# Kernel tuning notes

Hardware: AMD Instinct MI355X
Metric: run time of the kernel (lower is better)

## Reference

```python
import jax, jax.numpy as jnp
import numpy as np

B, S, D_MODEL, H, D_KV = 16, 512, 768, 12, 64
EPS = 1e-6
ROPE_THETA = 10000.0


def rms_norm(x, w, eps=EPS):
    var = jnp.mean(jnp.square(x.astype(jnp.float32)), axis=-1, keepdims=True)
    return w * (x * jax.lax.rsqrt(var + eps))


def rotate_half(x):
    x1, x2 = jnp.split(x, 2, axis=-1)
    return jnp.concatenate([-x2, x1], axis=-1)


def build_rope(position_ids, inv_freq):
    # position_ids: [B,S] int; inv_freq: [d_kv/2]
    freqs = position_ids[:, :, None].astype(jnp.float32) * inv_freq[None, None, :]  # [B,S,d/2]
    emb = jnp.concatenate([freqs, freqs], axis=-1)  # [B,S,d_kv]
    return jnp.cos(emb), jnp.sin(emb)


def shape_heads(x, n_heads, d_kv):
    b, s, _ = x.shape
    return x.reshape(b, s, n_heads, d_kv).transpose(0, 2, 1, 3)  # [b,h,s,d]


def attend(h, norm_w, wq, wk, wv, wo, mask, cos=None, sin=None):
    # h: [b,s,d_model]; mask: [b,h,s,s] additive
    normed = rms_norm(h, norm_w)
    q = shape_heads(normed @ wq.T, H, D_KV)
    k = shape_heads(normed @ wk.T, H, D_KV)
    v = shape_heads(normed @ wv.T, H, D_KV)
    if cos is not None:
        c = cos[:, None, :, :]
        s = sin[:, None, :, :]
        q = q * c + rotate_half(q) * s
        k = k * c + rotate_half(k) * s
    # NOTE: kernel has no 1/sqrt(d) scaling
    scores = jnp.einsum('bhqd,bhkd->bhqk', q, k) + mask
    p = jax.nn.softmax(scores, axis=-1)
    out = jnp.einsum('bhqk,bhkd->bhqd', p, v)
    b, _, s, _ = out.shape
    out = out.transpose(0, 2, 1, 3).reshape(b, s, H * D_KV)
    return h + out @ wo.T


def setup_inputs() -> dict:
    key = jax.random.key(0)
    ks = jax.random.split(key, 12)
    scale = 1.0 / np.sqrt(D_MODEL)
    inp = {
        'hidden_states': jax.random.normal(ks[0], (B, S, D_MODEL), dtype=jnp.float32),
        'position_ids': jnp.broadcast_to(jnp.arange(S, dtype=jnp.int32)[None, :], (B, S)),
        'attention_mask': jnp.broadcast_to(
            jnp.where(jnp.arange(S)[None, :] <= jnp.arange(S)[:, None], 0.0, -1e9).astype(jnp.float32),
            (B, H, S, S)) + 0.0,
        'group_time_mask': jnp.zeros((S, H, B, B), dtype=jnp.float32),
        't_q': jax.random.normal(ks[1], (H * D_KV, D_MODEL), dtype=jnp.float32) * scale,
        't_k': jax.random.normal(ks[2], (H * D_KV, D_MODEL), dtype=jnp.float32) * scale,
        't_v': jax.random.normal(ks[3], (H * D_KV, D_MODEL), dtype=jnp.float32) * scale,
        't_o': jax.random.normal(ks[4], (D_MODEL, H * D_KV), dtype=jnp.float32) * scale,
        't_norm_w': jnp.ones((D_MODEL,), dtype=jnp.float32),
        'g_q': jax.random.normal(ks[5], (H * D_KV, D_MODEL), dtype=jnp.float32) * scale,
        'g_k': jax.random.normal(ks[6], (H * D_KV, D_MODEL), dtype=jnp.float32) * scale,
        'g_v': jax.random.normal(ks[7], (H * D_KV, D_MODEL), dtype=jnp.float32) * scale,
        'g_o': jax.random.normal(ks[8], (D_MODEL, H * D_KV), dtype=jnp.float32) * scale,
        'g_norm_w': jnp.ones((D_MODEL,), dtype=jnp.float32),
        'inv_freq': (1.0 / ROPE_THETA ** (jnp.arange(0, D_KV, 2, dtype=jnp.float32) / D_KV)),
    }
    return inp


def reference(hidden_states, position_ids, attention_mask, group_time_mask,
              t_q, t_k, t_v, t_o, t_norm_w,
              g_q, g_k, g_v, g_o, g_norm_w, inv_freq):
    cos, sin = build_rope(position_ids, inv_freq)
    h = attend(hidden_states, t_norm_w, t_q, t_k, t_v, t_o, attention_mask, cos, sin)
    h = h.transpose(1, 0, 2)  # [S,B,D]: group attention attends across groups
    h = attend(h, g_norm_w, g_q, g_k, g_v, g_o, group_time_mask)
    return h.transpose(1, 0, 2)
```

## Files before the change

### kernel.cpp

```cpp
#include <hip/hip_runtime.h>

#define DM   768
#define QKVN 2304
#define SQ   512
#define NB   16
#define NH   12

typedef unsigned short u16;
typedef _Float16 h16;
typedef _Float16 h16x8 __attribute__((ext_vector_type(8)));
typedef float f32x4 __attribute__((ext_vector_type(4)));

__device__ __forceinline__ u16 f2h(float f) {
  h16 h = (h16)f;
  return __builtin_bit_cast(u16, h);
}
__device__ __forceinline__ float h2f(u16 u) {
  return (float)__builtin_bit_cast(h16, u);
}
__device__ __forceinline__ void gload_lds16(const void* g, void* l) {
  __builtin_amdgcn_global_load_lds((__attribute__((address_space(1))) void*)(g),
                                   (__attribute__((address_space(3))) void*)(l), 16, 0, 0);
}

struct WPtrs { const float* s[8]; u16* d[8]; };
__global__ __launch_bounds__(256) void prep_k(WPtrs P, const float* __restrict__ invf,
                                              float* __restrict__ tab,
                                              const float* __restrict__ x, const float* __restrict__ nw,
                                              u16* __restrict__ normed) {
  const int bid = blockIdx.x, tid = threadIdx.x;
  if (bid < 4608) {
    int w = bid / 576;
    int i = ((bid % 576) * 256 + tid) * 4;
    float4 v = *reinterpret_cast<const float4*>(P.s[w] + i);
    ushort4 o;
    o.x = f2h(v.x); o.y = f2h(v.y); o.z = f2h(v.z); o.w = f2h(v.w);
    *reinterpret_cast<ushort4*>(P.d[w] + i) = o;
  } else if (bid < 4672) {
    int i = (bid - 4608) * 256 + tid;
    int pos = i >> 5, j = i & 31;
    float a = (float)pos * invf[j];
    float s, c;
    sincosf(a, &s, &c);
    tab[i * 2] = c; tab[i * 2 + 1] = s;
  } else {
    int wv = tid >> 6, lane = tid & 63;
    size_t t = (size_t)(bid - 4672) * 4 + wv;
    const float* row = x + t * DM;
    float4 v[3];
    float ss = 0.f;
#pragma unroll
    for (int i = 0; i < 3; i++) {
      v[i] = *reinterpret_cast<const float4*>(row + (lane + 64 * i) * 4);
      ss += v[i].x * v[i].x + v[i].y * v[i].y + v[i].z * v[i].z + v[i].w * v[i].w;
    }
#pragma unroll
    for (int d = 1; d < 64; d <<= 1) ss += __shfl_xor(ss, d);
    float rs = rsqrtf(ss * (1.0f / 768.f) + 1e-6f);
    u16* orow = normed + t * DM;
#pragma unroll
    for (int i = 0; i < 3; i++) {
      int c = (lane + 64 * i) * 4;
      float4 wv4 = *reinterpret_cast<const float4*>(nw + c);
      ushort4 o;
      o.x = f2h(v[i].x * rs * wv4.x);
      o.y = f2h(v[i].y * rs * wv4.y);
      o.z = f2h(v[i].z * rs * wv4.z);
      o.w = f2h(v[i].w * rs * wv4.w);
      *reinterpret_cast<ushort4*>(orow + c) = o;
    }
  }
}

__global__ __launch_bounds__(256) void rms_k(const u16* __restrict__ x, const float* __restrict__ w,
                                             u16* __restrict__ out) {
  int wv = threadIdx.x >> 6, lane = threadIdx.x & 63;
  size_t t = (size_t)blockIdx.x * 4 + wv;
  const u16* row = x + t * DM;
  float4 v[3];
  float ss = 0.f;
#pragma unroll
  for (int i = 0; i < 3; i++) {
    ushort4 rw = *reinterpret_cast<const ushort4*>(row + (lane + 64 * i) * 4);
    v[i].x = h2f(rw.x); v[i].y = h2f(rw.y); v[i].z = h2f(rw.z); v[i].w = h2f(rw.w);
    ss += v[i].x * v[i].x + v[i].y * v[i].y + v[i].z * v[i].z + v[i].w * v[i].w;
  }
#pragma unroll
  for (int d = 1; d < 64; d <<= 1) ss += __shfl_xor(ss, d);
  float rs = rsqrtf(ss * (1.0f / 768.f) + 1e-6f);
  u16* orow = out + t * DM;
#pragma unroll
  for (int i = 0; i < 3; i++) {
    int c = (lane + 64 * i) * 4;
    float4 wv4 = *reinterpret_cast<const float4*>(w + c);
    ushort4 o;
    o.x = f2h(v[i].x * rs * wv4.x);
    o.y = f2h(v[i].y * rs * wv4.y);
    o.z = f2h(v[i].z * rs * wv4.z);
    o.w = f2h(v[i].w * rs * wv4.w);
    *reinterpret_cast<ushort4*>(orow + c) = o;
  }
}

template <int CMODE, bool ROPE, int PERM, bool VT>
__global__ __launch_bounds__(256, 3) void gemm_k(const u16* __restrict__ A, const u16* __restrict__ W, int N,
                                              void* __restrict__ C, const void* __restrict__ resid,
                                              const int* __restrict__ pids, const float* __restrict__ tab,
                                              u16* __restrict__ vt) {
  __shared__ __align__(16) char L[3 * 16384];
  const int tid = threadIdx.x, w = tid >> 6, lane = tid & 63;
  const int wr = w >> 1, wc = w & 1;
  const int nbn = gridDim.y;
  int nf = blockIdx.y * gridDim.x + blockIdx.x;
  int nwg = gridDim.x * nbn;
  int swv = (nf & 7) * (nwg >> 3) + (nf >> 3);
  const int bm = swv / nbn;
  const int bnb = swv % nbn;
  const int l15 = lane & 15, l4 = lane >> 4;
  f32x4 acc[4][4] = {};

  const int r0 = tid >> 2, k40 = tid & 3;
  const int k4s = k40 ^ ((r0 >> 1) & 3);
  const size_t aA0 = (size_t)(bm * 128 + r0) * 1536 + k4s * 16;
  const size_t aA1 = (size_t)(bm * 128 + r0 + 64) * 1536 + k4s * 16;
  const size_t aB0 = (size_t)(bnb * 128 + r0) * 1536 + k4s * 16;
  const size_t aB1 = (size_t)(bnb * 128 + r0 + 64) * 1536 + k4s * 16;
  const int dc0 = tid * 16, dc1 = dc0 + 4096;
  const char* Ab = (const char*)A;
  const char* Wb = (const char*)W;

#define STAGE(T64, Q) do { \
    gload_lds16(Ab + aA0 + (T64), L + (Q) * 16384 + dc0); \
    gload_lds16(Ab + aA1 + (T64), L + (Q) * 16384 + dc1); \
    gload_lds16(Wb + aB0 + (T64), L + (Q) * 16384 + 8192 + dc0); \
    gload_lds16(Wb + aB1 + (T64), L + (Q) * 16384 + 8192 + dc1); \
  } while (0)

  int obA[4], obB[4];
#pragma unroll
  for (int i = 0; i < 4; i++) {
    int rowA = wr * 64 + i * 16 + l15;
    obA[i] = rowA * 64 + ((l4 ^ ((rowA >> 1) & 3)) * 16);
    int rowB = wc * 64 + i * 16 + l15;
    obB[i] = 8192 + rowB * 64 + ((l4 ^ ((rowB >> 1) & 3)) * 16);
  }

  STAGE(0, 0); STAGE(64, 1);
  asm volatile("s_waitcnt vmcnt(4)" ::: "memory");
  __builtin_amdgcn_sched_barrier(0);
  __builtin_amdgcn_s_barrier();
  __builtin_amdgcn_sched_barrier(0);

#pragma unroll
  for (int to = 0; to < 8; ++to) {
#pragma unroll
    for (int ti = 0; ti < 3; ++ti) {
      const int t = to * 3 + ti;
      const int tn = (t + 2 < 24) ? (t + 2) : 23;
      STAGE(tn * 64, (t + 2) % 3);
      const char* bq = L + (t % 3) * 16384;
      h16x8 am[4], bn[4];
#pragma unroll
      for (int i = 0; i < 4; i++) am[i] = *reinterpret_cast<const h16x8*>(bq + obA[i]);
#pragma unroll
      for (int j = 0; j < 4; j++) bn[j] = *reinterpret_cast<const h16x8*>(bq + obB[j]);
      __builtin_amdgcn_s_setprio(1);
#pragma unroll
      for (int i = 0; i < 4; i++)
#pragma unroll
        for (int j = 0; j < 4; j++)
          acc[i][j] = __builtin_amdgcn_mfma_f32_16x16x32_f16(am[i], bn[j], acc[i][j], 0, 0, 0);
      __builtin_amdgcn_s_setprio(0);
      asm volatile("s_waitcnt vmcnt(4)" ::: "memory");
      __builtin_amdgcn_sched_barrier(0);
      __builtin_amdgcn_s_barrier();
      __builtin_amdgcn_sched_barrier(0);
    }
  }
#undef STAGE
  asm volatile("s_waitcnt vmcnt(0)" ::: "memory");

  if (VT && bnb >= 12) {
#pragma unroll
    for (int i = 0; i < 4; i++) {
      int row0 = bm * 128 + wr * 64 + i * 16 + l4 * 4;
      int b = row0 >> 9, s0 = row0 & 511;
#pragma unroll
      for (int j = 0; j < 4; j++) {
        int vcol = bnb * 128 + wc * 64 + j * 16 + l15 - 1536;
        int hh = vcol >> 6, dd = vcol & 63;
        u16* dst = vt + (((size_t)(b * NH + hh) * 64 + dd) << 9) + s0;
        ushort4 o;
        o.x = f2h(acc[i][j][0]); o.y = f2h(acc[i][j][1]);
        o.z = f2h(acc[i][j][2]); o.w = f2h(acc[i][j][3]);
        *reinterpret_cast<ushort4*>(dst) = o;
      }
    }
    return;
  }

  if (ROPE && bnb < 12) {
#pragma unroll
    for (int i = 0; i < 4; i++) {
      int row0 = bm * 128 + wr * 64 + i * 16 + l4 * 4;
#pragma unroll
      for (int r = 0; r < 4; r++) {
        int pos = pids[row0 + r];
        const float* tb = tab + pos * 64;
#pragma unroll
        for (int j = 0; j < 2; j++) {
          float2 cs = *reinterpret_cast<const float2*>(tb + 2 * (j * 16 + l15));
          float x1 = acc[i][j][r], x2 = acc[i][j + 2][r];
          acc[i][j][r]     = x1 * cs.x - x2 * cs.y;
          acc[i][j + 2][r] = x2 * cs.x + x1 * cs.y;
        }
      }
    }
  }
#pragma unroll
  for (int i = 0; i < 4; i++) {
    int row0 = bm * 128 + wr * 64 + i * 16 + l4 * 4;
#pragma unroll
    for (int j = 0; j < 4; j++) {
      int col = bnb * 128 + wc * 64 + j * 16 + l15;
#pragma unroll
      for (int r = 0; r < 4; r++) {
        int rr = row0 + r;
        int orow = (PERM == 0) ? rr : (PERM == 1) ? ((rr & 511) * 16 + (rr >> 9))
                                                  : ((rr & 15) * 512 + (rr >> 4));
        size_t idx = (size_t)orow * N + col;
        float v = acc[i][j][r];
        if (CMODE == 0)      ((u16*)C)[idx] = f2h(v);
        else if (CMODE == 1) ((u16*)C)[idx] = f2h(v + ((const float*)resid)[idx]);
        else                 ((float*)C)[idx] = v + h2f(((const u16*)resid)[idx]);
      }
    }
  }
}

__global__ __launch_bounds__(256) void attn1_k(const u16* __restrict__ qkv, const u16* __restrict__ vt,
                                               u16* __restrict__ O) {
  __shared__ __align__(16) char L[2][32768];
  __shared__ __align__(16) char Pl[4][4096];
  const int qt = blockIdx.x;
  const int bh = blockIdx.y;
  const int b = bh / NH, h = bh % NH;
  const int tid = threadIdx.x, w = tid >> 6, lane = tid & 63;
  const int l15 = lane & 15, l4 = lane >> 4;
  const size_t qoff = ((size_t)(b * SQ + qt * 64 + w * 16 + l15)) * QKVN + h * 64;
  h16x8 qf[2];
  qf[0] = *reinterpret_cast<const h16x8*>(qkv + qoff + 8 * l4);
  qf[1] = *reinterpret_cast<const h16x8*>(qkv + qoff + 32 + 8 * l4);
  f32x4 acco[4] = {};
  float mrun[4] = {-3e38f, -3e38f, -3e38f, -3e38f};
  float lrun[4] = {0.f, 0.f, 0.f, 0.f};
  const int qrow = qt * 64 + w * 16 + l4 * 4;
  const int nkt = (qt >> 1) + 1;

  const u16* Kg = qkv + (size_t)b * SQ * QKVN + DM + h * 64;
  const int rK0 = tid >> 3;
  const size_t aK0 = (size_t)rK0 * QKVN + (size_t)(((tid & 7) ^ (rK0 & 7)) * 8);
  const u16* Vg = vt + (size_t)bh * 64 * SQ;
  const int dV0 = tid >> 4;
  const size_t aV0 = (size_t)dV0 * SQ + (size_t)(((tid & 15) ^ (dV0 & 15)) * 8);
  const int dst0 = tid * 16;

#define STAGE1(KT, BUF) do { \
    _Pragma("unroll") \
    for (int e = 0; e < 4; e++) \
      gload_lds16(Kg + aK0 + (size_t)e * (32 * QKVN) + (size_t)(KT) * (128 * QKVN), \
                  L[BUF] + dst0 + e * 4096); \
    _Pragma("unroll") \
    for (int e = 0; e < 4; e++) \
      gload_lds16(Vg + aV0 + e * (16 * SQ) + (KT) * 128, \
                  L[BUF] + 16384 + dst0 + e * 4096); \
  } while (0)

  STAGE1(0, 0);
  asm volatile("s_waitcnt vmcnt(0)" ::: "memory");
  __builtin_amdgcn_sched_barrier(0);
  __builtin_amdgcn_s_barrier();
  __builtin_amdgcn_sched_barrier(0);

  for (int kt = 0; kt < nkt; ++kt) {
    const int cur = kt & 1;
    if (kt + 1 < nkt) STAGE1(kt + 1, cur ^ 1);
    const char* Kb = L[cur];
    const char* Vb = L[cur] + 16384;
    f32x4 sc[8] = {};
    __builtin_amdgcn_s_setprio(1);
#pragma unroll
    for (int kk = 0; kk < 2; kk++) {
#pragma unroll
      for (int j = 0; j < 8; j++) {
        int row = j * 16 + l15;
        int off = row * 128 + (((kk * 4 + l4) ^ (row & 7)) * 16);
        h16x8 kf = *reinterpret_cast<const h16x8*>(Kb + off);
        sc[j] = __builtin_amdgcn_mfma_f32_16x16x32_f16(qf[kk], kf, sc[j], 0, 0, 0);
      }
    }
    __builtin_amdgcn_s_setprio(0);
    float pv[8][4];
#pragma unroll
    for (int j = 0; j < 8; j++)
#pragma unroll
      for (int r = 0; r < 4; r++) pv[j][r] = sc[j][r];
    if (kt == nkt - 1) {
#pragma unroll
      for (int r = 0; r < 4; r++) {
        int q = qrow + r;
#pragma unroll
        for (int j = 0; j < 8; j++) {
          int key = kt * 128 + j * 16 + l15;
          if (key > q) pv[j][r] = -1e30f;
        }
      }
    }
    float al[4];
#pragma unroll
    for (int r = 0; r < 4; r++) {
      float t0 = fmaxf(fmaxf(pv[0][r], pv[1][r]), fmaxf(pv[2][r], pv[3][r]));
      float t1 = fmaxf(fmaxf(pv[4][r], pv[5][r]), fmaxf(pv[6][r], pv[7][r]));
      float tm = fmaxf(t0, t1);
      tm = fmaxf(tm, __shfl_xor(tm, 1)); tm = fmaxf(tm, __shfl_xor(tm, 2));
      tm = fmaxf(tm, __shfl_xor(tm, 4)); tm = fmaxf(tm, __shfl_xor(tm, 8));
      float mn = fmaxf(mrun[r], tm);
      al[r] = __expf(mrun[r] - mn);
      mrun[r] = mn;
      float ts = 0.f;
#pragma unroll
      for (int j = 0; j < 8; j++) { float p = __expf(pv[j][r] - mn); pv[j][r] = p; ts += p; }
      ts += __shfl_xor(ts, 1); ts += __shfl_xor(ts, 2); ts += __shfl_xor(ts, 4); ts += __shfl_xor(ts, 8);
      lrun[r] = lrun[r] * al[r] + ts;
    }
#pragma unroll
    for (int j = 0; j < 4; j++)
#pragma unroll
      for (int r = 0; r < 4; r++) acco[j][r] *= al[r];
    char* pw = Pl[w];
#pragma unroll
    for (int r = 0; r < 4; r++) {
      int q = l4 * 4 + r;
#pragma unroll
      for (int j = 0; j < 8; j++) {
        int cw = j * 2 + (l15 >> 3);
        int byte = q * 256 + ((cw ^ (q & 15)) * 16) + (l15 & 7) * 2;
        *(u16*)(pw + byte) = f2h(pv[j][r]);
      }
    }
    asm volatile("s_waitcnt lgkmcnt(0)" ::: "memory");
    __builtin_amdgcn_sched_barrier(0);
    __builtin_amdgcn_s_setprio(1);
#pragma unroll
    for (int kk = 0; kk < 4; kk++) {
      h16x8 pa = *reinterpret_cast<const h16x8*>(pw + l15 * 256 + (((kk * 4 + l4) ^ l15) * 16));
#pragma unroll
      for (int j = 0; j < 4; j++) {
        int d = j * 16 + l15;
        int voff = d * 256 + (((kk * 4 + l4) ^ (d & 15)) * 16);
        h16x8 vf = *reinterpret_cast<const h16x8*>(Vb + voff);
        acco[j] = __builtin_amdgcn_mfma_f32_16x16x32_f16(pa, vf, acco[j], 0, 0, 0);
      }
    }
    __builtin_amdgcn_s_setprio(0);
    asm volatile("s_waitcnt vmcnt(0)" ::: "memory");
    __builtin_amdgcn_sched_barrier(0);
    __builtin_amdgcn_s_barrier();
    __builtin_amdgcn_sched_barrier(0);
  }
#undef STAGE1
#pragma unroll
  for (int r = 0; r < 4; r++) {
    float inv = 1.f / lrun[r];
    size_t orow = ((size_t)(b * SQ + qrow + r)) * DM + h * 64;
#pragma unroll
    for (int j = 0; j < 4; j++) O[orow + j * 16 + l15] = f2h(acco[j][r] * inv);
  }
}

__global__ __launch_bounds__(256) void attn2_k(const u16* __restrict__ qkv, const float* __restrict__ gmask,
                                               u16* __restrict__ O) {
  __shared__ float Pl[4][16][16];
  __shared__ float Vl[4][16][68];
  const int tid = threadIdx.x, w = tid >> 6, lane = tid & 63;
  const int idx = blockIdx.x * 4 + w;
  const int s = idx / NH, h = idx % NH;
  const int l15 = lane & 15, l4 = lane >> 4;
  const size_t base = ((size_t)(s * 16 + l15)) * QKVN + h * 64;
  h16x8 qf0 = *reinterpret_cast<const h16x8*>(qkv + base + 8 * l4);
  h16x8 qf1 = *reinterpret_cast<const h16x8*>(qkv + base + 32 + 8 * l4);
  h16x8 kf0 = *reinterpret_cast<const h16x8*>(qkv + base + DM + 8 * l4);
  h16x8 kf1 = *reinterpret_cast<const h16x8*>(qkv + base + DM + 32 + 8 * l4);
  f32x4 sc = {};
  sc = __builtin_amdgcn_mfma_f32_16x16x32_f16(qf0, kf0, sc, 0, 0, 0);
  sc = __builtin_amdgcn_mfma_f32_16x16x32_f16(qf1, kf1, sc, 0, 0, 0);
  {
    int key = lane >> 2, d0 = (lane & 3) * 16;
    const u16* vsrc = qkv + ((size_t)(s * 16 + key)) * QKVN + 2 * DM + h * 64 + d0;
#pragma unroll
    for (int i = 0; i < 16; i += 4) {
      ushort4 vv = *reinterpret_cast<const ushort4*>(vsrc + i);
      Vl[w][key][d0 + i + 0] = h2f(vv.x);
      Vl[w][key][d0 + i + 1] = h2f(vv.y);
      Vl[w][key][d0 + i + 2] = h2f(vv.z);
      Vl[w][key][d0 + i + 3] = h2f(vv.w);
    }
  }
  const float* gm = gmask + ((size_t)s * NH + h) * 256;
#pragma unroll
  for (int r = 0; r < 4; r++) {
    float v = sc[r] + gm[(l4 * 4 + r) * 16 + l15];
    float mx = v;
    mx = fmaxf(mx, __shfl_xor(mx, 1)); mx = fmaxf(mx, __shfl_xor(mx, 2));
    mx = fmaxf(mx, __shfl_xor(mx, 4)); mx = fmaxf(mx, __shfl_xor(mx, 8));
    float p = __expf(v - mx);
    float su = p;
    su += __shfl_xor(su, 1); su += __shfl_xor(su, 2); su += __shfl_xor(su, 4); su += __shfl_xor(su, 8);
    Pl[w][l4 * 4 + r][l15] = p / su;
  }
  asm volatile("s_waitcnt lgkmcnt(0)" ::: "memory");
  __builtin_amdgcn_sched_barrier(0);
  const int q = lane >> 2, d0 = (lane & 3) * 16;
  float o[16] = {};
#pragma unroll
  for (int key = 0; key < 16; key++) {
    float pp = Pl[w][q][key];
#pragma unroll
    for (int dd = 0; dd < 16; dd += 4) {
      float4 vv = *reinterpret_cast<const float4*>(&Vl[w][key][d0 + dd]);
      o[dd + 0] += pp * vv.x; o[dd + 1] += pp * vv.y; o[dd + 2] += pp * vv.z; o[dd + 3] += pp * vv.w;
    }
  }
  u16* orow = O + ((size_t)(s * 16 + q)) * DM + h * 64 + d0;
#pragma unroll
  for (int i = 0; i < 16; i += 4) {
    ushort4 ov;
    ov.x = f2h(o[i]); ov.y = f2h(o[i + 1]); ov.z = f2h(o[i + 2]); ov.w = f2h(o[i + 3]);
    *reinterpret_cast<ushort4*>(orow + i) = ov;
  }
}

extern "C" void kernel_launch(void* const* d_in, const int* in_sizes, int n_in,
                              void* d_out, int out_size, void* d_ws, size_t ws_size,
                              hipStream_t stream) {
  const float* hidden = (const float*)d_in[0];
  const int*   pids   = (const int*)d_in[1];
  const float* gmask  = (const float*)d_in[3];
  const float* tq = (const float*)d_in[4];
  const float* tk = (const float*)d_in[5];
  const float* tv = (const float*)d_in[6];
  const float* to_ = (const float*)d_in[7];
  const float* tnw = (const float*)d_in[8];
  const float* gq = (const float*)d_in[9];
  const float* gk = (const float*)d_in[10];
  const float* gv = (const float*)d_in[11];
  const float* go = (const float*)d_in[12];
  const float* gnw = (const float*)d_in[13];
  const float* invf = (const float*)d_in[14];
  float* out = (float*)d_out;
  char* ws = (char*)d_ws;

  u16*   wq1    = (u16*)(ws);
  u16*   wo1    = (u16*)(ws + 3538944);
  u16*   wq2    = (u16*)(ws + 4718592);
  u16*   wo2    = (u16*)(ws + 8257536);
  float* tab    = (float*)(ws + 9437184);
  u16*   normed = (u16*)(ws + 9568256);
  u16*   obuf   = (u16*)(ws + 22151168);
  u16*   h1     = (u16*)(ws + 34734080);
  u16*   qkv    = (u16*)(ws + 59899904);
  u16*   vt     = (u16*)(ws + 97648640);

  const int WN = 768 * 768;
  WPtrs P;
  P.s[0] = tq;  P.d[0] = wq1;
  P.s[1] = tk;  P.d[1] = wq1 + WN;
  P.s[2] = tv;  P.d[2] = wq1 + 2 * WN;
  P.s[3] = to_; P.d[3] = wo1;
  P.s[4] = gq;  P.d[4] = wq2;
  P.s[5] = gk;  P.d[5] = wq2 + WN;
  P.s[6] = gv;  P.d[6] = wq2 + 2 * WN;
  P.s[7] = go;  P.d[7] = wo2;

  prep_k<<<6720, 256, 0, stream>>>(P, invf, tab, hidden, tnw, normed);
  gemm_k<0, true, 0, true><<<dim3(64, 18), 256, 0, stream>>>(normed, wq1, QKVN, qkv, nullptr, pids, tab, vt);
  attn1_k<<<dim3(8, 192), 256, 0, stream>>>(qkv, vt, obuf);
  gemm_k<1, false, 0, false><<<dim3(64, 6), 256, 0, stream>>>(obuf, wo1, DM, h1, hidden, nullptr, nullptr, nullptr);

  rms_k<<<2048, 256, 0, stream>>>(h1, gnw, normed);
  gemm_k<0, false, 1, false><<<dim3(64, 18), 256, 0, stream>>>(normed, wq2, QKVN, qkv, nullptr, nullptr, nullptr, nullptr);
  attn2_k<<<1536, 256, 0, stream>>>(qkv, gmask, obuf);
  gemm_k<2, false, 2, false><<<dim3(64, 6), 256, 0, stream>>>(obuf, wo2, DM, out, h1, nullptr, nullptr, nullptr);
}
```

Baseline: 206.3 us.

## Fold RMSNorm weights into QKV weights and apply row scale in GEMM epilogue

```diff
diff --git a/kernel.cpp b/kernel.cpp
--- a/kernel.cpp
+++ b/kernel.cpp
@@ -26,13 +26,20 @@
 struct WPtrs { const float* s[8]; u16* d[8]; };
 __global__ __launch_bounds__(256) void prep_k(WPtrs P, const float* __restrict__ invf,
                                               float* __restrict__ tab,
-                                              const float* __restrict__ x, const float* __restrict__ nw,
-                                              u16* __restrict__ normed) {
+                                              const float* __restrict__ x,
+                                              const float* __restrict__ tnw, const float* __restrict__ gnw,
+                                              u16* __restrict__ xh, float* __restrict__ rs1) {
   const int bid = blockIdx.x, tid = threadIdx.x;
   if (bid < 4608) {
     int w = bid / 576;
     int i = ((bid % 576) * 256 + tid) * 4;
     float4 v = *reinterpret_cast<const float4*>(P.s[w] + i);
+    if (w < 3 || (w >= 4 && w < 7)) {
+      const float* nw = (w < 3) ? tnw : gnw;
+      int k = i % 768;
+      float4 f = *reinterpret_cast<const float4*>(nw + k);
+      v.x *= f.x; v.y *= f.y; v.z *= f.z; v.w *= f.w;
+    }
     ushort4 o;
     o.x = f2h(v.x); o.y = f2h(v.y); o.z = f2h(v.z); o.w = f2h(v.w);
     *reinterpret_cast<ushort4*>(P.d[w] + i) = o;
@@ -56,57 +63,39 @@
     }
 #pragma unroll
     for (int d = 1; d < 64; d <<= 1) ss += __shfl_xor(ss, d);
-    float rs = rsqrtf(ss * (1.0f / 768.f) + 1e-6f);
-    u16* orow = normed + t * DM;
+    u16* orow = xh + t * DM;
 #pragma unroll
     for (int i = 0; i < 3; i++) {
       int c = (lane + 64 * i) * 4;
-      float4 wv4 = *reinterpret_cast<const float4*>(nw + c);
       ushort4 o;
-      o.x = f2h(v[i].x * rs * wv4.x);
-      o.y = f2h(v[i].y * rs * wv4.y);
-      o.z = f2h(v[i].z * rs * wv4.z);
-      o.w = f2h(v[i].w * rs * wv4.w);
+      o.x = f2h(v[i].x); o.y = f2h(v[i].y); o.z = f2h(v[i].z); o.w = f2h(v[i].w);
       *reinterpret_cast<ushort4*>(orow + c) = o;
     }
-  }
-}
-
-__global__ __launch_bounds__(256) void rms_k(const u16* __restrict__ x, const float* __restrict__ w,
-                                             u16* __restrict__ out) {
+    if (lane == 0) rs1[t] = rsqrtf(ss * (1.0f / 768.f) + 1e-6f);
+  }
+}
+
+__global__ __launch_bounds__(256) void rs2_k(const u16* __restrict__ x, float* __restrict__ rs2) {
   int wv = threadIdx.x >> 6, lane = threadIdx.x & 63;
   size_t t = (size_t)blockIdx.x * 4 + wv;
   const u16* row = x + t * DM;
-  float4 v[3];
   float ss = 0.f;
 #pragma unroll
   for (int i = 0; i < 3; i++) {
     ushort4 rw = *reinterpret_cast<const ushort4*>(row + (lane + 64 * i) * 4);
-    v[i].x = h2f(rw.x); v[i].y = h2f(rw.y); v[i].z = h2f(rw.z); v[i].w = h2f(rw.w);
-    ss += v[i].x * v[i].x + v[i].y * v[i].y + v[i].z * v[i].z + v[i].w * v[i].w;
+    float a = h2f(rw.x), b = h2f(rw.y), c = h2f(rw.z), d = h2f(rw.w);
+    ss += a * a + b * b + c * c + d * d;
   }
 #pragma unroll
   for (int d = 1; d < 64; d <<= 1) ss += __shfl_xor(ss, d);
-  float rs = rsqrtf(ss * (1.0f / 768.f) + 1e-6f);
-  u16* orow = out + t * DM;
-#pragma unroll
-  for (int i = 0; i < 3; i++) {
-    int c = (lane + 64 * i) * 4;
-    float4 wv4 = *reinterpret_cast<const float4*>(w + c);
-    ushort4 o;
-    o.x = f2h(v[i].x * rs * wv4.x);
-    o.y = f2h(v[i].y * rs * wv4.y);
-    o.z = f2h(v[i].z * rs * wv4.z);
-    o.w = f2h(v[i].w * rs * wv4.w);
-    *reinterpret_cast<ushort4*>(orow + c) = o;
-  }
-}
-
-template <int CMODE, bool ROPE, int PERM, bool VT>
+  if (lane == 0) rs2[t] = rsqrtf(ss * (1.0f / 768.f) + 1e-6f);
+}
+
+template <int CMODE, bool ROPE, int PERM, bool VT, bool RS>
 __global__ __launch_bounds__(256, 3) void gemm_k(const u16* __restrict__ A, const u16* __restrict__ W, int N,
                                               void* __restrict__ C, const void* __restrict__ resid,
                                               const int* __restrict__ pids, const float* __restrict__ tab,
-                                              u16* __restrict__ vt) {
+                                              u16* __restrict__ vt, const float* __restrict__ rsb) {
   __shared__ __align__(16) char L[3 * 16384];
   const int tid = threadIdx.x, w = tid >> 6, lane = tid & 63;
   const int wr = w >> 1, wc = w & 1;
@@ -180,6 +169,19 @@
 #undef STAGE
   asm volatile("s_waitcnt vmcnt(0)" ::: "memory");
 
+  if (RS) {
+#pragma unroll
+    for (int i = 0; i < 4; i++) {
+      int row0 = bm * 128 + wr * 64 + i * 16 + l4 * 4;
+#pragma unroll
+      for (int r = 0; r < 4; r++) {
+        float s = rsb[row0 + r];
+#pragma unroll
+        for (int j = 0; j < 4; j++) acc[i][j][r] *= s;
+      }
+    }
+  }
+
   if (VT && bnb >= 12) {
 #pragma unroll
     for (int i = 0; i < 4; i++) {
@@ -231,7 +233,7 @@
         size_t idx = (size_t)orow * N + col;
         float v = acc[i][j][r];
         if (CMODE == 0)      ((u16*)C)[idx] = f2h(v);
-        else if (CMODE == 1) ((u16*)C)[idx] = f2h(v + ((const float*)resid)[idx]);
+        else if (CMODE == 1) ((u16*)C)[idx] = f2h(v + h2f(((const u16*)resid)[idx]));
         else                 ((float*)C)[idx] = v + h2f(((const u16*)resid)[idx]);
       }
     }
@@ -242,8 +244,10 @@
                                                u16* __restrict__ O) {
   __shared__ __align__(16) char L[2][32768];
   __shared__ __align__(16) char Pl[4][4096];
-  const int qt = blockIdx.x;
-  const int bh = blockIdx.y;
+  int nf = blockIdx.y * 8 + blockIdx.x;
+  int swv = (nf & 7) * 192 + (nf >> 3);
+  const int qt = swv & 7;
+  const int bh = swv >> 3;
   const int b = bh / NH, h = bh % NH;
   const int tid = threadIdx.x, w = tid >> 6, lane = tid & 63;
   const int l15 = lane & 15, l4 = lane >> 4;
@@ -465,11 +469,13 @@
   u16*   wq2    = (u16*)(ws + 4718592);
   u16*   wo2    = (u16*)(ws + 8257536);
   float* tab    = (float*)(ws + 9437184);
-  u16*   normed = (u16*)(ws + 9568256);
+  u16*   xh     = (u16*)(ws + 9568256);
   u16*   obuf   = (u16*)(ws + 22151168);
   u16*   h1     = (u16*)(ws + 34734080);
   u16*   qkv    = (u16*)(ws + 59899904);
   u16*   vt     = (u16*)(ws + 97648640);
+  float* rs1    = (float*)(ws + 110231552);
+  float* rs2    = (float*)(ws + 110264320);
 
   const int WN = 768 * 768;
   WPtrs P;
@@ -482,13 +488,13 @@
   P.s[6] = gv;  P.d[6] = wq2 + 2 * WN;
   P.s[7] = go;  P.d[7] = wo2;
 
-  prep_k<<<6720, 256, 0, stream>>>(P, invf, tab, hidden, tnw, normed);
-  gemm_k<0, true, 0, true><<<dim3(64, 18), 256, 0, stream>>>(normed, wq1, QKVN, qkv, nullptr, pids, tab, vt);
+  prep_k<<<6720, 256, 0, stream>>>(P, invf, tab, hidden, tnw, gnw, xh, rs1);
+  gemm_k<0, true, 0, true, true><<<dim3(64, 18), 256, 0, stream>>>(xh, wq1, QKVN, qkv, nullptr, pids, tab, vt, rs1);
   attn1_k<<<dim3(8, 192), 256, 0, stream>>>(qkv, vt, obuf);
-  gemm_k<1, false, 0, false><<<dim3(64, 6), 256, 0, stream>>>(obuf, wo1, DM, h1, hidden, nullptr, nullptr, nullptr);
-
-  rms_k<<<2048, 256, 0, stream>>>(h1, gnw, normed);
-  gemm_k<0, false, 1, false><<<dim3(64, 18), 256, 0, stream>>>(normed, wq2, QKVN, qkv, nullptr, nullptr, nullptr, nullptr);
+  gemm_k<1, false, 0, false, false><<<dim3(64, 6), 256, 0, stream>>>(obuf, wo1, DM, h1, xh, nullptr, nullptr, nullptr, nullptr);
+
+  rs2_k<<<2048, 256, 0, stream>>>(h1, rs2);
+  gemm_k<0, false, 1, false, true><<<dim3(64, 18), 256, 0, stream>>>(h1, wq2, QKVN, qkv, nullptr, nullptr, nullptr, nullptr, rs2);
   attn2_k<<<1536, 256, 0, stream>>>(qkv, gmask, obuf);
-  gemm_k<2, false, 2, false><<<dim3(64, 6), 256, 0, stream>>>(obuf, wo2, DM, out, h1, nullptr, nullptr, nullptr);
-}
+  gemm_k<2, false, 2, false, false><<<dim3(64, 6), 256, 0, stream>>>(obuf, wo2, DM, out, h1, nullptr, nullptr, nullptr, nullptr);
+}
```

Measured after the change: 197.0 us. 1.05x faster.
